# Kernel tuning notes

Hardware: AMD Instinct MI355X
Metric: run time of the kernel (lower is better)

Reference implementation:

```python
import jax, jax.numpy as jnp
import numpy as np

B, S, D, H = 2, 2048, 1024, 16
HD = D // H  # head_dim = 64


def setup_inputs() -> dict:
    key = jax.random.key(0)
    ks = jax.random.split(key, 9)
    s_in = 1.0 / np.sqrt(D)
    inp = {
        "hidden_state": jax.random.normal(ks[0], (B, S, D), dtype=jnp.float32),
        # per-head projections, stacked: [H, D, HD]
        "Wq": jax.random.uniform(ks[1], (H, D, HD), jnp.float32, -s_in, s_in),
        "bq": jax.random.uniform(ks[2], (H, HD), jnp.float32, -s_in, s_in),
        "Wk": jax.random.uniform(ks[3], (H, D, HD), jnp.float32, -s_in, s_in),
        "bk": jax.random.uniform(ks[4], (H, HD), jnp.float32, -s_in, s_in),
        "Wv": jax.random.uniform(ks[5], (H, D, HD), jnp.float32, -s_in, s_in),
        "bv": jax.random.uniform(ks[6], (H, HD), jnp.float32, -s_in, s_in),
        # output linear: [D, D]
        "Wo": jax.random.uniform(ks[7], (D, D), jnp.float32, -s_in, s_in),
        "bo": jax.random.uniform(ks[8], (D,), jnp.float32, -s_in, s_in),
    }
    return inp


def reference(hidden_state, Wq, bq, Wk, bk, Wv, bv, Wo, bo):
    # fused per-head projections: [B, H, S, HD]
    q = jnp.einsum("bsd,hde->bhse", hidden_state, Wq) + bq[None, :, None, :]
    k = jnp.einsum("bsd,hde->bhse", hidden_state, Wk) + bk[None, :, None, :]
    v = jnp.einsum("bsd,hde->bhse", hidden_state, Wv) + bv[None, :, None, :]
    scale = 1.0 / jnp.sqrt(jnp.float32(HD))
    scores = jnp.einsum("bhse,bhte->bhst", q, k) * scale  # [B, H, S, S]
    weights = jax.nn.softmax(scores, axis=-1)
    ctx = jnp.einsum("bhst,bhte->bhse", weights, v)       # [B, H, S, HD]
    # concat heads along last dim -> [B, S, D]
    ctx = jnp.transpose(ctx, (0, 2, 1, 3)).reshape(B, S, D)
    return ctx @ Wo + bo
```

## Files before the change

### kernel.cpp

```cpp
#include <hip/hip_runtime.h>
#include <hip/hip_bf16.h>
#include <math.h>

#define BB 2
#define SS 2048
#define DD 1024
#define HH 16
#define HD 64

typedef __attribute__((ext_vector_type(8))) _Float16 f16x8;
typedef __attribute__((ext_vector_type(2))) __fp16 fp16x2;
typedef __attribute__((ext_vector_type(8))) unsigned short u16x8;
typedef __attribute__((ext_vector_type(4))) float f32x4;
typedef __attribute__((ext_vector_type(4))) unsigned short u16x4;

__device__ __forceinline__ unsigned short hbits(_Float16 h) {
    union { _Float16 h; unsigned short s; } u; u.h = h; return u.s;
}

__device__ __forceinline__ int swz(int row, int grp) {
    return (row << 6) + (((grp) ^ (row & 7)) << 3);
}

__device__ __forceinline__ float fexp2(float x) {
#if __has_builtin(__builtin_amdgcn_exp2f)
    return __builtin_amdgcn_exp2f(x);
#else
    return exp2f(x);
#endif
}

__device__ __forceinline__ u16x4 pack4(float p0, float p1, float p2, float p3) {
#if __has_builtin(__builtin_amdgcn_cvt_pkrtz)
    union { fp16x2 h[2]; u16x4 u; } pu;
    pu.h[0] = __builtin_amdgcn_cvt_pkrtz(p0, p1);
    pu.h[1] = __builtin_amdgcn_cvt_pkrtz(p2, p3);
    return pu.u;
#else
    u16x4 r;
    r[0] = hbits((_Float16)p0); r[1] = hbits((_Float16)p1);
    r[2] = hbits((_Float16)p2); r[3] = hbits((_Float16)p3);
    return r;
#endif
}

__device__ __forceinline__ void gload_lds16(const unsigned short* g, unsigned short* l) {
#if __has_builtin(__builtin_amdgcn_global_load_lds)
    auto gp = (const __attribute__((address_space(1))) unsigned int*)(uintptr_t)g;
    auto lp = (__attribute__((address_space(3))) unsigned int*)(uintptr_t)l;
    __builtin_amdgcn_global_load_lds(gp, lp, 16, 0, 0);
#else
    *(u16x8*)(l + (threadIdx.x & 63) * 8) = *(const u16x8*)g;
#endif
}

__global__ __launch_bounds__(256) void prep_convert(
    const float* __restrict__ X,
    const float* __restrict__ Wq, const float* __restrict__ Wk,
    const float* __restrict__ Wv, const float* __restrict__ Wo,
    unsigned short* __restrict__ Xh, unsigned short* __restrict__ WT)
{
    __shared__ __align__(16) unsigned short LT[64 * 68];
    const int bid = blockIdx.x;
    const int tid = threadIdx.x;

    if (bid < 2048) {
        const int base = bid * 2048 + tid * 8;
        float4 a = *(const float4*)&X[base];
        float4 b = *(const float4*)&X[base + 4];
        u16x8 o;
        o[0] = hbits((_Float16)a.x); o[1] = hbits((_Float16)a.y);
        o[2] = hbits((_Float16)a.z); o[3] = hbits((_Float16)a.w);
        o[4] = hbits((_Float16)b.x); o[5] = hbits((_Float16)b.y);
        o[6] = hbits((_Float16)b.z); o[7] = hbits((_Float16)b.w);
        *(u16x8*)&Xh[base] = o;
        return;
    }

    const int t = bid - 2048;
    const float* src;
    size_t stride;
    int outRow0, kcol0;
    if (t < 768) {
        const int nt = t >> 4, ktile = t & 15;
        const int sel = nt >> 4, hh = nt & 15;
        const float* Ws = (sel == 0) ? Wq : ((sel == 1) ? Wk : Wv);
        src = Ws + (size_t)hh * (DD * HD) + (size_t)ktile * 64 * HD;
        stride = HD;
        outRow0 = nt * 64;
        kcol0 = ktile * 64;
    } else {
        const int tt = t - 768;
        const int nt = tt & 15, ktile = tt >> 4;
        src = Wo + (size_t)ktile * 64 * DD + nt * 64;
        stride = DD;
        outRow0 = 3072 + nt * 64;
        kcol0 = ktile * 64;
    }

    const int e = tid & 63, dq = tid >> 6;
#pragma unroll
    for (int p = 0; p < 16; p++) {
        const int dl = p * 4 + dq;
        LT[e * 68 + dl] = hbits((_Float16)src[(size_t)dl * stride + e]);
    }
    __syncthreads();
    const int eo = tid >> 2, d16 = (tid & 3) * 16;
#pragma unroll
    for (int j = 0; j < 4; j++) {
        *(ushort4*)&WT[(size_t)(outRow0 + eo) * DD + kcol0 + d16 + j * 4] =
            *(const ushort4*)&LT[eo * 68 + d16 + j * 4];
    }
}

#define GBM 128
#define GBN 128
#define GBK 64
#define NKT (DD / GBK)
#define QBK 32
#define QNKT (DD / QBK)

__global__ __launch_bounds__(256) void qkv_gemm(
    const unsigned short* __restrict__ Xh, const unsigned short* __restrict__ WT,
    const float* __restrict__ bq, const float* __restrict__ bk,
    const float* __restrict__ bv,
    unsigned short* __restrict__ qh, unsigned short* __restrict__ kh,
    unsigned short* __restrict__ vTs, unsigned int* __restrict__ kc2)
{
    __shared__ __align__(16) unsigned short As[2][8 * 512];
    __shared__ __align__(16) unsigned short Bs[2][8 * 512];

    const int tid = threadIdx.x;
    const int m0 = blockIdx.y * GBM;
    const int n0 = blockIdx.x * GBN;
    const int lane = tid & 63;
    const int w = tid >> 6;
    const int wm = w & 1, wn = w >> 1;
    const int l15 = lane & 15, quad = lane >> 4;

    int g_off[2];
#pragma unroll
    for (int p = 0; p < 2; p++) {
        const int c = p * 4 + w;
        g_off[p] = (c * 16 + l15) * DD + quad * 8;
    }

    f32x4 acc[4][4];
#pragma unroll
    for (int i = 0; i < 4; i++)
#pragma unroll
        for (int j = 0; j < 4; j++) acc[i][j] = (f32x4){0.f, 0.f, 0.f, 0.f};

    const unsigned short* Abase = Xh + (size_t)m0 * DD;
    const unsigned short* Bbase = WT + (size_t)n0 * DD;

#pragma unroll
    for (int p = 0; p < 2; p++) {
        gload_lds16(Abase + g_off[p], &As[0][(p * 4 + w) * 512]);
        gload_lds16(Bbase + g_off[p], &Bs[0][(p * 4 + w) * 512]);
    }

    for (int it = 0; it < QNKT; it++) {
        const int cur = it & 1;
        __syncthreads();
        if (it + 1 < QNKT) {
            const int kt2 = (it + 1) * QBK;
#pragma unroll
            for (int p = 0; p < 2; p++) {
                gload_lds16(Abase + g_off[p] + kt2, &As[cur ^ 1][(p * 4 + w) * 512]);
                gload_lds16(Bbase + g_off[p] + kt2, &Bs[cur ^ 1][(p * 4 + w) * 512]);
            }
        }
        f16x8 af[4], bf[4];
#pragma unroll
        for (int i = 0; i < 4; i++) {
            af[i] = *(const f16x8*)&As[cur][(wm * 4 + i) * 512 + lane * 8];
            bf[i] = *(const f16x8*)&Bs[cur][(wn * 4 + i) * 512 + lane * 8];
        }
#pragma unroll
        for (int ns = 0; ns < 4; ns++)
#pragma unroll
            for (int ms = 0; ms < 4; ms++)
                acc[ms][ns] = __builtin_amdgcn_mfma_f32_16x16x32_f16(
                    af[ms], bf[ns], acc[ms][ns], 0, 0, 0);
    }

    const int sel = n0 >> 10;
    const int hw = ((n0 + wn * 64) >> 6) & 15;
    const int bblk = m0 >> 11;
    const float* bias = (sel == 0) ? bq : ((sel == 1) ? bk : bv);
    const size_t bh_base = ((size_t)bblk * HH + hw) * SS * HD;
    float wmx = 0.0f;
#pragma unroll
    for (int ms = 0; ms < 4; ms++) {
#pragma unroll
        for (int rr = 0; rr < 4; rr++) {
            const int m = m0 + wm * 64 + ms * 16 + quad * 4 + rr;
            const int s = m & (SS - 1);
            const int s63 = s & 63;
            float v2 = 0.0f;
#pragma unroll
            for (int ns = 0; ns < 4; ns++) {
                const int e = ns * 16 + l15;
                const float val = acc[ms][ns][rr] + bias[hw * HD + e];
                if (sel == 0) {
                    qh[bh_base + (size_t)s * HD + e] = hbits((_Float16)val);
                } else if (sel == 1) {
                    v2 = fmaf(val, val, v2);
                    const size_t kofs = bh_base + (size_t)(s >> 6) * 4096
                                      + swz(s63, e >> 3) + (e & 7);
                    kh[kofs] = hbits((_Float16)val);
                } else {
                    const size_t vofs = bh_base + (size_t)(s >> 6) * 4096
                                      + swz(e, s63 >> 3) + (s63 & 7);
                    vTs[vofs] = hbits((_Float16)val);
                }
            }
            if (sel == 1) {
                v2 += __shfl_xor(v2, 1);
                v2 += __shfl_xor(v2, 2);
                v2 += __shfl_xor(v2, 4);
                v2 += __shfl_xor(v2, 8);
                wmx = fmaxf(wmx, v2);
            }
        }
    }
    if (sel == 1) {
        wmx = fmaxf(wmx, __shfl_xor(wmx, 16));
        wmx = fmaxf(wmx, __shfl_xor(wmx, 32));
        if (lane == 0)
            atomicMax(&kc2[bblk * HH + hw], __float_as_uint(wmx));
    }
}

__global__ __launch_bounds__(256) void out_gemm(
    const unsigned short* __restrict__ Ctxh, const unsigned short* __restrict__ WoT,
    const float* __restrict__ bo, float* __restrict__ out)
{
    __shared__ __align__(16) unsigned short As[2][16 * 512];
    __shared__ __align__(16) unsigned short Bs[2][16 * 512];

    const int tid = threadIdx.x;
    const int m0 = blockIdx.y * GBM;
    const int n0 = blockIdx.x * GBN;
    const int lane = tid & 63;
    const int w = tid >> 6;
    const int wm = w & 1, wn = w >> 1;
    const int l15 = lane & 15, quad = lane >> 4;

    int g_off[4];
#pragma unroll
    for (int p = 0; p < 4; p++) {
        const int c = p * 4 + w;
        g_off[p] = ((c >> 1) * 16 + (lane & 15)) * DD + (c & 1) * 32 + (lane >> 4) * 8;
    }

    f32x4 acc[4][4];
#pragma unroll
    for (int i = 0; i < 4; i++)
#pragma unroll
        for (int j = 0; j < 4; j++) acc[i][j] = (f32x4){0.f, 0.f, 0.f, 0.f};

    const unsigned short* Abase = Ctxh + (size_t)m0 * DD;
    const unsigned short* Bbase = WoT + (size_t)n0 * DD;

#pragma unroll
    for (int p = 0; p < 4; p++) {
        gload_lds16(Abase + g_off[p], &As[0][(p * 4 + w) * 512]);
        gload_lds16(Bbase + g_off[p], &Bs[0][(p * 4 + w) * 512]);
    }

    for (int it = 0; it < NKT; it++) {
        const int cur = it & 1;
        __syncthreads();
        if (it + 1 < NKT) {
            const int kt2 = (it + 1) * GBK;
#pragma unroll
            for (int p = 0; p < 4; p++) {
                gload_lds16(Abase + g_off[p] + kt2, &As[cur ^ 1][(p * 4 + w) * 512]);
                gload_lds16(Bbase + g_off[p] + kt2, &Bs[cur ^ 1][(p * 4 + w) * 512]);
            }
        }
#pragma unroll
        for (int ks = 0; ks < 2; ks++) {
            f16x8 af[4], bf[4];
#pragma unroll
            for (int i = 0; i < 4; i++) {
                af[i] = *(const f16x8*)&As[cur][((wm * 4 + i) * 2 + ks) * 512 + lane * 8];
                bf[i] = *(const f16x8*)&Bs[cur][((wn * 4 + i) * 2 + ks) * 512 + lane * 8];
            }
#pragma unroll
            for (int ns = 0; ns < 4; ns++)
#pragma unroll
                for (int ms = 0; ms < 4; ms++)
                    acc[ms][ns] = __builtin_amdgcn_mfma_f32_16x16x32_f16(
                        af[ms], bf[ns], acc[ms][ns], 0, 0, 0);
        }
    }

#pragma unroll
    for (int ms = 0; ms < 4; ms++) {
#pragma unroll
        for (int rr = 0; rr < 4; rr++) {
            const size_t m = (size_t)(m0 + wm * 64 + ms * 16 + quad * 4 + rr);
#pragma unroll
            for (int ns = 0; ns < 4; ns++) {
                const int n = n0 + wn * 64 + ns * 16 + l15;
                out[m * DD + n] = acc[ms][ns][rr] + bo[n];
            }
        }
    }
}

#define TQB 128
#define TKB 64
#define NT (SS / TKB)
#define C1 0.1803368801111204f

__global__ __launch_bounds__(256) void attn_mfma(
    const unsigned short* __restrict__ qh, const unsigned short* __restrict__ kh,
    const unsigned short* __restrict__ vTs, const unsigned int* __restrict__ kc2,
    unsigned short* __restrict__ ctxh)
{
    __shared__ __align__(16) unsigned short KL [2][TKB * 64];
    __shared__ __align__(16) unsigned short VtL[2][HD * 64];
    __shared__ __align__(16) unsigned short PsL[4][32 * 64];

    const int tid  = threadIdx.x;
    const int lane = tid & 63;
    const int w    = tid >> 6;
    const int l15  = lane & 15;
    const int quad = lane >> 4;
    const int bh   = blockIdx.y;
    const int q0   = blockIdx.x * TQB;

    const float kfac = sqrtf(__uint_as_float(kc2[bh])) * 1.01f * C1;

    f16x8 qf[2][2];
    float M2[2];
#pragma unroll
    for (int msub = 0; msub < 2; msub++) {
        const unsigned short* qrow =
            qh + ((size_t)bh * SS + q0 + w * 32 + msub * 16 + l15) * HD;
        float nq2 = 0.0f;
#pragma unroll
        for (int dstep = 0; dstep < 2; dstep++) {
            qf[msub][dstep] = *(const f16x8*)&qrow[dstep * 32 + quad * 8];
#pragma unroll
            for (int j = 0; j < 8; j++) {
                const float x = (float)qf[msub][dstep][j];
                nq2 = fmaf(x, x, nq2);
            }
        }
        nq2 += __shfl_xor(nq2, 16);
        nq2 += __shfl_xor(nq2, 32);
        M2[msub] = sqrtf(nq2) * kfac;
    }

    f16x8 ones;
#pragma unroll
    for (int j = 0; j < 8; j++) ones[j] = (_Float16)1.0f;

    f32x4 o[2][4], lones[2];
#pragma unroll
    for (int ms = 0; ms < 2; ms++) {
        lones[ms] = (f32x4){0.f, 0.f, 0.f, 0.f};
#pragma unroll
        for (int e = 0; e < 4; e++) o[ms][e] = (f32x4){0.f, 0.f, 0.f, 0.f};
    }

    const unsigned short* kb0 = kh  + (size_t)bh * SS * HD;
    const unsigned short* vb0 = vTs + (size_t)bh * SS * HD;

    gload_lds16(kb0 + tid * 8,        &KL [0][w * 512]);
    gload_lds16(kb0 + 2048 + tid * 8, &KL [0][2048 + w * 512]);
    gload_lds16(vb0 + tid * 8,        &VtL[0][w * 512]);
    gload_lds16(vb0 + 2048 + tid * 8, &VtL[0][2048 + w * 512]);

    for (int t = 0; t < NT; t++) {
        const int cur = t & 1;
        __syncthreads();
        if (t + 1 < NT) {
            const unsigned short* kb = kb0 + (size_t)(t + 1) * 4096;
            const unsigned short* vb = vb0 + (size_t)(t + 1) * 4096;
            gload_lds16(kb + tid * 8,        &KL [cur ^ 1][w * 512]);
            gload_lds16(kb + 2048 + tid * 8, &KL [cur ^ 1][2048 + w * 512]);
            gload_lds16(vb + tid * 8,        &VtL[cur ^ 1][w * 512]);
            gload_lds16(vb + 2048 + tid * 8, &VtL[cur ^ 1][2048 + w * 512]);
        }

        f32x4 sc[2][4];
#pragma unroll
        for (int ksub = 0; ksub < 4; ksub++) {
            const int row = ksub * 16 + l15;
            f16x8 k0 = *(const f16x8*)&KL[cur][swz(row, quad)];
            f16x8 k1 = *(const f16x8*)&KL[cur][swz(row, 4 + quad)];
#pragma unroll
            for (int msub = 0; msub < 2; msub++) {
                f32x4 a = (f32x4){0.f, 0.f, 0.f, 0.f};
                a = __builtin_amdgcn_mfma_f32_16x16x32_f16(k0, qf[msub][0], a, 0, 0, 0);
                a = __builtin_amdgcn_mfma_f32_16x16x32_f16(k1, qf[msub][1], a, 0, 0, 0);
                sc[msub][ksub] = a;
            }
        }

#pragma unroll
        for (int msub = 0; msub < 2; msub++) {
            const int prow = msub * 16 + l15;
#pragma unroll
            for (int ksub = 0; ksub < 4; ksub++) {
                const float p0 = fexp2(fmaf(sc[msub][ksub][0], C1, -M2[msub]));
                const float p1 = fexp2(fmaf(sc[msub][ksub][1], C1, -M2[msub]));
                const float p2 = fexp2(fmaf(sc[msub][ksub][2], C1, -M2[msub]));
                const float p3 = fexp2(fmaf(sc[msub][ksub][3], C1, -M2[msub]));
                *(u16x4*)&PsL[w][swz(prow, ksub * 2 + (quad >> 1)) + (quad & 1) * 4] =
                    pack4(p0, p1, p2, p3);
            }
        }

#pragma unroll
        for (int kj = 0; kj < 2; kj++) {
            f16x8 pa[2];
#pragma unroll
            for (int msub = 0; msub < 2; msub++)
                pa[msub] = *(const f16x8*)&PsL[w][swz(msub * 16 + l15, kj * 4 + quad)];
            lones[0] = __builtin_amdgcn_mfma_f32_16x16x32_f16(pa[0], ones, lones[0], 0, 0, 0);
            lones[1] = __builtin_amdgcn_mfma_f32_16x16x32_f16(pa[1], ones, lones[1], 0, 0, 0);
#pragma unroll
            for (int esub = 0; esub < 4; esub++) {
                f16x8 vr = *(const f16x8*)&VtL[cur][swz(esub * 16 + l15, kj * 4 + quad)];
                o[0][esub] = __builtin_amdgcn_mfma_f32_16x16x32_f16(pa[0], vr, o[0][esub], 0, 0, 0);
                o[1][esub] = __builtin_amdgcn_mfma_f32_16x16x32_f16(pa[1], vr, o[1][esub], 0, 0, 0);
            }
        }
    }

    const int b = bh >> 4;
    const int h = bh & 15;
#pragma unroll
    for (int msub = 0; msub < 2; msub++) {
#pragma unroll
        for (int rr = 0; rr < 4; rr++) {
            const float linv = 1.0f / lones[msub][rr];
            const int row = q0 + w * 32 + msub * 16 + quad * 4 + rr;
#pragma unroll
            for (int esub = 0; esub < 4; esub++) {
                ctxh[((size_t)b * SS + row) * DD + h * HD + esub * 16 + l15] =
                    hbits((_Float16)(o[msub][esub][rr] * linv));
            }
        }
    }
}

extern "C" void kernel_launch(void* const* d_in, const int* in_sizes, int n_in,
                              void* d_out, int out_size, void* d_ws, size_t ws_size,
                              hipStream_t stream) {
    const float* X  = (const float*)d_in[0];
    const float* Wq = (const float*)d_in[1];
    const float* bq = (const float*)d_in[2];
    const float* Wk = (const float*)d_in[3];
    const float* bk = (const float*)d_in[4];
    const float* Wv = (const float*)d_in[5];
    const float* bv = (const float*)d_in[6];
    const float* Wo = (const float*)d_in[7];
    const float* bo = (const float*)d_in[8];
    float* out = (float*)d_out;

    const size_t NB2 = (size_t)4096 * 1024 * 2;
    unsigned char* w8 = (unsigned char*)d_ws;
    unsigned short* Xh   = (unsigned short*)(w8);
    unsigned short* WT   = (unsigned short*)(w8 + NB2);
    unsigned short* qh   = (unsigned short*)(w8 + 2 * NB2);
    unsigned short* kh   = (unsigned short*)(w8 + 3 * NB2);
    unsigned short* vTs  = (unsigned short*)(w8 + 4 * NB2);
    unsigned short* ctxh = (unsigned short*)(w8 + 5 * NB2);
    unsigned int*   kc2  = (unsigned int*)(w8 + 6 * NB2);
    unsigned short* WoT  = WT + (size_t)3072 * 1024;

    (void)hipMemsetAsync(kc2, 0, BB * HH * sizeof(unsigned int), stream);

    prep_convert<<<dim3(3072), 256, 0, stream>>>(X, Wq, Wk, Wv, Wo, Xh, WT);

    qkv_gemm<<<dim3(3072 / GBN, 4096 / GBM), 256, 0, stream>>>(
        Xh, WT, bq, bk, bv, qh, kh, vTs, kc2);

    attn_mfma<<<dim3(SS / TQB, BB * HH), 256, 0, stream>>>(qh, kh, vTs, kc2, ctxh);

    out_gemm<<<dim3(1024 / GBN, 4096 / GBM), 256, 0, stream>>>(ctxh, WoT, bo, out);
}
```

Before: 232.4 us.

## Triple-buffer LDS tiles with partial vmcnt waits in GEMM and attention kernels

Converts the double-buffered global-to-LDS pipelines in the QKV GEMM, output GEMM and attention kernels to triple buffering with a prefetch distance of two tiles. The per-iteration __syncthreads is replaced by inline-asm s_waitcnt vmcnt(N) plus s_barrier, so only the oldest tile's loads must land before the next compute step. This aims to hide more global-load latency. It costs about 1.5x the LDS for these buffers, which may lower occupancy, and it relies on exact hand-counted vmcnt values.

Measured after the change: 220.5 us. -5.1%, faster.

```diff
diff --git a/kernel.cpp b/kernel.cpp
--- a/kernel.cpp
+++ b/kernel.cpp
@@ -52,6 +52,16 @@
 #else
     *(u16x8*)(l + (threadIdx.x & 63) * 8) = *(const u16x8*)g;
 #endif
+}
+
+__device__ __forceinline__ void wait4_barrier() {
+    asm volatile("s_waitcnt vmcnt(4) lgkmcnt(0)\n\ts_barrier" ::: "memory");
+}
+__device__ __forceinline__ void wait8_barrier() {
+    asm volatile("s_waitcnt vmcnt(8) lgkmcnt(0)\n\ts_barrier" ::: "memory");
+}
+__device__ __forceinline__ void wait0_barrier() {
+    asm volatile("s_waitcnt vmcnt(0) lgkmcnt(0)\n\ts_barrier" ::: "memory");
 }
 
 __global__ __launch_bounds__(256) void prep_convert(
@@ -127,8 +137,8 @@
     unsigned short* __restrict__ qh, unsigned short* __restrict__ kh,
     unsigned short* __restrict__ vTs, unsigned int* __restrict__ kc2)
 {
-    __shared__ __align__(16) unsigned short As[2][8 * 512];
-    __shared__ __align__(16) unsigned short Bs[2][8 * 512];
+    __shared__ __align__(16) unsigned short As[3][8 * 512];
+    __shared__ __align__(16) unsigned short Bs[3][8 * 512];
 
     const int tid = threadIdx.x;
     const int m0 = blockIdx.y * GBM;
@@ -159,16 +169,21 @@
         gload_lds16(Abase + g_off[p], &As[0][(p * 4 + w) * 512]);
         gload_lds16(Bbase + g_off[p], &Bs[0][(p * 4 + w) * 512]);
     }
-
-    for (int it = 0; it < QNKT; it++) {
-        const int cur = it & 1;
-        __syncthreads();
-        if (it + 1 < QNKT) {
-            const int kt2 = (it + 1) * QBK;
+#pragma unroll
+    for (int p = 0; p < 2; p++) {
+        gload_lds16(Abase + g_off[p] + QBK, &As[1][(p * 4 + w) * 512]);
+        gload_lds16(Bbase + g_off[p] + QBK, &Bs[1][(p * 4 + w) * 512]);
+    }
+    wait0_barrier();
+
+    int cur = 0, pre = 2;
+    for (int t = 0; t < QNKT; t++) {
+        if (t + 2 < QNKT) {
+            const int kt2 = (t + 2) * QBK;
 #pragma unroll
             for (int p = 0; p < 2; p++) {
-                gload_lds16(Abase + g_off[p] + kt2, &As[cur ^ 1][(p * 4 + w) * 512]);
-                gload_lds16(Bbase + g_off[p] + kt2, &Bs[cur ^ 1][(p * 4 + w) * 512]);
+                gload_lds16(Abase + g_off[p] + kt2, &As[pre][(p * 4 + w) * 512]);
+                gload_lds16(Bbase + g_off[p] + kt2, &Bs[pre][(p * 4 + w) * 512]);
             }
         }
         f16x8 af[4], bf[4];
@@ -183,6 +198,10 @@
             for (int ms = 0; ms < 4; ms++)
                 acc[ms][ns] = __builtin_amdgcn_mfma_f32_16x16x32_f16(
                     af[ms], bf[ns], acc[ms][ns], 0, 0, 0);
+        if (t < QNKT - 2)       wait4_barrier();
+        else if (t == QNKT - 2) wait0_barrier();
+        cur = (cur == 2) ? 0 : cur + 1;
+        pre = (pre == 2) ? 0 : pre + 1;
     }
 
     const int sel = n0 >> 10;
@@ -237,8 +256,8 @@
     const unsigned short* __restrict__ Ctxh, const unsigned short* __restrict__ WoT,
     const float* __restrict__ bo, float* __restrict__ out)
 {
-    __shared__ __align__(16) unsigned short As[2][16 * 512];
-    __shared__ __align__(16) unsigned short Bs[2][16 * 512];
+    __shared__ __align__(16) unsigned short As[3][16 * 512];
+    __shared__ __align__(16) unsigned short Bs[3][16 * 512];
 
     const int tid = threadIdx.x;
     const int m0 = blockIdx.y * GBM;
@@ -269,16 +288,21 @@
         gload_lds16(Abase + g_off[p], &As[0][(p * 4 + w) * 512]);
         gload_lds16(Bbase + g_off[p], &Bs[0][(p * 4 + w) * 512]);
     }
-
+#pragma unroll
+    for (int p = 0; p < 4; p++) {
+        gload_lds16(Abase + g_off[p] + GBK, &As[1][(p * 4 + w) * 512]);
+        gload_lds16(Bbase + g_off[p] + GBK, &Bs[1][(p * 4 + w) * 512]);
+    }
+    wait0_barrier();
+
+    int cur = 0, pre = 2;
     for (int it = 0; it < NKT; it++) {
-        const int cur = it & 1;
-        __syncthreads();
-        if (it + 1 < NKT) {
-            const int kt2 = (it + 1) * GBK;
+        if (it + 2 < NKT) {
+            const int kt2 = (it + 2) * GBK;
 #pragma unroll
             for (int p = 0; p < 4; p++) {
-                gload_lds16(Abase + g_off[p] + kt2, &As[cur ^ 1][(p * 4 + w) * 512]);
-                gload_lds16(Bbase + g_off[p] + kt2, &Bs[cur ^ 1][(p * 4 + w) * 512]);
+                gload_lds16(Abase + g_off[p] + kt2, &As[pre][(p * 4 + w) * 512]);
+                gload_lds16(Bbase + g_off[p] + kt2, &Bs[pre][(p * 4 + w) * 512]);
             }
         }
 #pragma unroll
@@ -296,6 +320,10 @@
                     acc[ms][ns] = __builtin_amdgcn_mfma_f32_16x16x32_f16(
                         af[ms], bf[ns], acc[ms][ns], 0, 0, 0);
         }
+        if (it < NKT - 2)       wait8_barrier();
+        else if (it == NKT - 2) wait0_barrier();
+        cur = (cur == 2) ? 0 : cur + 1;
+        pre = (pre == 2) ? 0 : pre + 1;
     }
 
 #pragma unroll
@@ -322,8 +350,8 @@
     const unsigned short* __restrict__ vTs, const unsigned int* __restrict__ kc2,
     unsigned short* __restrict__ ctxh)
 {
-    __shared__ __align__(16) unsigned short KL [2][TKB * 64];
-    __shared__ __align__(16) unsigned short VtL[2][HD * 64];
+    __shared__ __align__(16) unsigned short KL [3][TKB * 64];
+    __shared__ __align__(16) unsigned short VtL[3][HD * 64];
     __shared__ __align__(16) unsigned short PsL[4][32 * 64];
 
     const int tid  = threadIdx.x;
@@ -376,17 +404,21 @@
     gload_lds16(kb0 + 2048 + tid * 8, &KL [0][2048 + w * 512]);
     gload_lds16(vb0 + tid * 8,        &VtL[0][w * 512]);
     gload_lds16(vb0 + 2048 + tid * 8, &VtL[0][2048 + w * 512]);
-
+    gload_lds16(kb0 + 4096 + tid * 8, &KL [1][w * 512]);
+    gload_lds16(kb0 + 6144 + tid * 8, &KL [1][2048 + w * 512]);
+    gload_lds16(vb0 + 4096 + tid * 8, &VtL[1][w * 512]);
+    gload_lds16(vb0 + 6144 + tid * 8, &VtL[1][2048 + w * 512]);
+    wait0_barrier();
+
+    int cur = 0, pre = 2;
     for (int t = 0; t < NT; t++) {
-        const int cur = t & 1;
-        __syncthreads();
-        if (t + 1 < NT) {
-            const unsigned short* kb = kb0 + (size_t)(t + 1) * 4096;
-            const unsigned short* vb = vb0 + (size_t)(t + 1) * 4096;
-            gload_lds16(kb + tid * 8,        &KL [cur ^ 1][w * 512]);
-            gload_lds16(kb + 2048 + tid * 8, &KL [cur ^ 1][2048 + w * 512]);
-            gload_lds16(vb + tid * 8,        &VtL[cur ^ 1][w * 512]);
-            gload_lds16(vb + 2048 + tid * 8, &VtL[cur ^ 1][2048 + w * 512]);
+        if (t + 2 < NT) {
+            const unsigned short* kb = kb0 + (size_t)(t + 2) * 4096;
+            const unsigned short* vb = vb0 + (size_t)(t + 2) * 4096;
+            gload_lds16(kb + tid * 8,        &KL [pre][w * 512]);
+            gload_lds16(kb + 2048 + tid * 8, &KL [pre][2048 + w * 512]);
+            gload_lds16(vb + tid * 8,        &VtL[pre][w * 512]);
+            gload_lds16(vb + 2048 + tid * 8, &VtL[pre][2048 + w * 512]);
         }
 
         f32x4 sc[2][4];
@@ -433,6 +465,11 @@
                 o[1][esub] = __builtin_amdgcn_mfma_f32_16x16x32_f16(pa[1], vr, o[1][esub], 0, 0, 0);
             }
         }
+
+        if (t < NT - 2)       wait4_barrier();
+        else if (t == NT - 2) wait0_barrier();
+        cur = (cur == 2) ? 0 : cur + 1;
+        pre = (pre == 2) ? 0 : pre + 1;
     }
 
     const int b = bh >> 4;
```
